# Kernel optimization log

Measured on AMD Instinct MI355X. Metric: run time of the kernel, lower is better.

## Reference

```python
import jax, jax.numpy as jnp
import numpy as np

HEADS = 16

def _rope(x):
    # x: (B, H, T, D); rotate pairs (even, odd) along last dim, positions along axis 2
    B, H, T, D = x.shape
    half = D // 2
    theta = 10000.0 ** (-jnp.arange(half, dtype=x.dtype) / half)          # (half,)
    angles = jnp.arange(T, dtype=x.dtype)[:, None] * theta                # (T, half)
    sin, cos = jnp.sin(angles), jnp.cos(angles)                           # (T, half)
    x1, x2 = x[..., ::2], x[..., 1::2]                                    # (B,H,T,half)
    rot = jnp.stack([x1 * cos - x2 * sin, x1 * sin + x2 * cos], axis=-1)  # (B,H,T,half,2)
    return rot.reshape(B, H, T, D)

def setup_inputs() -> dict:
    key = jax.random.key(0)
    k1, k2, k3 = jax.random.split(key, 3)
    B, T, C = 2, 2048, 1024
    return {
        "x": jax.random.normal(k1, (B, T, C), dtype=jnp.float32),
        "W_qkv": jax.random.normal(k2, (3 * C, C), dtype=jnp.float32) * 0.02,
        "W_out": jax.random.normal(k3, (C, C), dtype=jnp.float32) * 0.02,
        "window": 256,
    }

def reference(x, W_qkv, W_out, window):
    B, T, C = x.shape
    H = HEADS
    D = C // H
    # fused QKV projection (torch Linear: y = x @ W.T)
    qkv = jnp.einsum('btc,fc->btf', x, W_qkv)            # (B,T,3C)
    qkv = qkv.reshape(B, T, H, 3 * D).transpose(0, 2, 1, 3)  # (B,H,T,3D)
    q, k, v = jnp.split(qkv, 3, axis=-1)                 # each (B,H,T,D)
    q, k = _rope(q), _rope(k)
    # causal + local-window boolean mask: allow j in [i-window, i]
    i = jnp.arange(T)[:, None]
    j = jnp.arange(T)[None, :]
    mask = (j <= i) & (j >= i - window)                  # (T,T) bool
    scale = 1.0 / jnp.sqrt(jnp.asarray(D, dtype=x.dtype))
    scores = jnp.einsum('bhqd,bhkd->bhqk', q, k) * scale # (B,H,T,T)
    scores = jnp.where(mask[None, None], scores, -jnp.inf)
    attn = jax.nn.softmax(scores, axis=-1)
    out = jnp.einsum('bhqk,bhkd->bhqd', attn, v)         # (B,H,T,D)
    out = out.transpose(0, 2, 1, 3).reshape(B, T, C)
    return jnp.einsum('btc,oc->bto', out, W_out)
```

## Files before the change

### kernel.cpp

```cpp
#include <hip/hip_runtime.h>

typedef float f32x4 __attribute__((ext_vector_type(4)));
typedef __bf16 bf16x8 __attribute__((ext_vector_type(8)));
typedef unsigned short u16x4 __attribute__((ext_vector_type(4)));

__device__ __forceinline__ unsigned short f2bf(float f) {
  union { float f; unsigned int u; } v; v.f = f;
  unsigned int r = (v.u + 0x7FFFu + ((v.u >> 16) & 1u)) >> 16;
  return (unsigned short)r;
}
__device__ __forceinline__ float bf2f(unsigned short h) {
  union { unsigned int u; float f; } v; v.u = ((unsigned int)h) << 16;
  return v.f;
}
__device__ __forceinline__ void gload_lds16(const void* g, void* l) {
  __builtin_amdgcn_global_load_lds(
      (const __attribute__((address_space(1))) unsigned int*)g,
      (__attribute__((address_space(3))) unsigned int*)l, 16, 0, 0);
}

__global__ __launch_bounds__(256) void f2bf_kernel(const float* __restrict__ in,
                                                   unsigned short* __restrict__ out,
                                                   int n4) {
  int i = blockIdx.x * 256 + threadIdx.x;
  if (i < n4) {
    float4 v = ((const float4*)in)[i];
    u16x4 o;
    o.x = f2bf(v.x); o.y = f2bf(v.y); o.z = f2bf(v.z); o.w = f2bf(v.w);
    ((u16x4*)out)[i] = o;
  }
}

template <bool OUTBF16>
__global__ __launch_bounds__(256) void gemm_bt(const unsigned short* __restrict__ A,
                                               const unsigned short* __restrict__ B,
                                               void* __restrict__ C,
                                               int M, int N, int K) {
  __shared__ unsigned short As[128][32];
  __shared__ unsigned short Bs[128][32];
  const int tid = threadIdx.x;
  const int lane = tid & 63;
  const int w = tid >> 6, wr = w >> 1, wc = w & 1;
  const int bm = blockIdx.y * 128, bn = blockIdx.x * 128;
  const int t4 = tid >> 2, c8 = (tid & 3) * 8;
  const unsigned short* Ab = A + (size_t)(bm + t4) * K + c8;
  const unsigned short* Bb = B + (size_t)(bn + t4) * K + c8;
  const int rq = lane & 15, kg = (lane >> 4) * 8;
  f32x4 acc[4][4] = {};
  for (int kt = 0; kt < K; kt += 32) {
    gload_lds16(Ab + kt,                  &As[t4][c8]);
    gload_lds16(Ab + kt + (size_t)64 * K, &As[t4 + 64][c8]);
    gload_lds16(Bb + kt,                  &Bs[t4][c8]);
    gload_lds16(Bb + kt + (size_t)64 * K, &Bs[t4 + 64][c8]);
    __syncthreads();
    bf16x8 fa[4], fb[4];
#pragma unroll
    for (int m = 0; m < 4; ++m) fa[m] = *(const bf16x8*)&As[wr * 64 + m * 16 + rq][kg];
#pragma unroll
    for (int n = 0; n < 4; ++n) fb[n] = *(const bf16x8*)&Bs[wc * 64 + n * 16 + rq][kg];
#pragma unroll
    for (int m = 0; m < 4; ++m)
#pragma unroll
      for (int n = 0; n < 4; ++n)
        acc[m][n] = __builtin_amdgcn_mfma_f32_16x16x32_bf16(fa[m], fb[n], acc[m][n], 0, 0, 0);
    __syncthreads();
  }
  const int r0 = bm + wr * 64 + (lane >> 4) * 4;
  const int c0 = bn + wc * 64 + rq;
#pragma unroll
  for (int m = 0; m < 4; ++m)
#pragma unroll
    for (int n = 0; n < 4; ++n)
#pragma unroll
      for (int j = 0; j < 4; ++j) {
        int row = r0 + m * 16 + j, col = c0 + n * 16;
        if (OUTBF16)
          ((unsigned short*)C)[(size_t)row * N + col] = f2bf(acc[m][n][j]);
        else
          ((float*)C)[(size_t)row * N + col] = acc[m][n][j];
      }
}

__global__ __launch_bounds__(256) void rope_inplace(unsigned short* __restrict__ qkv) {
  int idx = blockIdx.x * 256 + threadIdx.x;
  int dp = idx & 31;
  int t  = (idx >> 5) & 2047;
  int bh = idx >> 16;
  int b = bh >> 4, h = bh & 15;
  unsigned short* p = qkv + (size_t)(b * 2048 + t) * 3072 + h * 192 + dp * 2;
  float theta = exp2f(-(float)dp * 0.4152410118609203f);
  float ang = (float)t * theta;
  float sn, cs;
  sincosf(ang, &sn, &cs);
  float q1 = bf2f(p[0]), q2 = bf2f(p[1]);
  p[0] = f2bf(q1 * cs - q2 * sn);
  p[1] = f2bf(q1 * sn + q2 * cs);
  float k1 = bf2f(p[64]), k2 = bf2f(p[65]);
  p[64] = f2bf(k1 * cs - k2 * sn);
  p[65] = f2bf(k1 * sn + k2 * cs);
}

#define WMAX 256
__global__ __launch_bounds__(256) void attn_kernel(const unsigned short* __restrict__ qkv,
                                                   unsigned short* __restrict__ attnb,
                                                   const int* __restrict__ winp) {
  __shared__ unsigned short Qs[64][72];
  __shared__ unsigned short KPs[320 * 72];
  __shared__ unsigned short Vt[64][328];
  const int T = 2048;
  const int tid = threadIdx.x;
  const int bid = blockIdx.x;
  const int qt = bid & 31;
  const int bh = bid >> 5;
  const int b = bh >> 4, h = bh & 15;
  const int qbase = qt * 64;
  const int kbase = qbase - WMAX;
  const int win = *winp;
  const unsigned short* base = qkv + (size_t)b * T * 3072 + h * 192;
  const int tr = tid >> 2, tc = (tid & 3) * 16;
  {
    const unsigned short* s = base + (size_t)(qbase + tr) * 3072 + tc;
    *(int4*)&Qs[tr][tc]     = *(const int4*)s;
    *(int4*)&Qs[tr][tc + 8] = *(const int4*)(s + 8);
  }
#pragma unroll
  for (int p5 = 0; p5 < 5; ++p5) {
    int s = p5 * 64 + tr;
    int j = kbase + s;
    int jc = j < 0 ? 0 : j;
    const unsigned short* sk = base + (size_t)jc * 3072 + 64 + tc;
    *(int4*)&KPs[s * 72 + tc]     = *(const int4*)sk;
    *(int4*)&KPs[s * 72 + tc + 8] = *(const int4*)(sk + 8);
    const unsigned short* sv = base + (size_t)jc * 3072 + 128 + tc;
    unsigned short tmp[16];
    *(int4*)&tmp[0] = *(const int4*)sv;
    *(int4*)&tmp[8] = *(const int4*)(sv + 8);
#pragma unroll
    for (int e = 0; e < 16; ++e) Vt[tc + e][s] = tmp[e];
  }
  __syncthreads();
  const int lane = tid & 63, wv = tid >> 6;
  const int rbase = wv * 16;
  const int rq = lane & 15, kg = (lane >> 4) * 8;
  bf16x8 qa[2];
#pragma unroll
  for (int kk = 0; kk < 2; ++kk)
    qa[kk] = *(const bf16x8*)&Qs[rbase + rq][kk * 32 + kg];
  float sc[20][4];
#pragma unroll
  for (int n = 0; n < 20; ++n) {
    f32x4 s = {};
#pragma unroll
    for (int kk = 0; kk < 2; ++kk) {
      bf16x8 kb = *(const bf16x8*)&KPs[(n * 16 + rq) * 72 + kk * 32 + kg];
      s = __builtin_amdgcn_mfma_f32_16x16x32_bf16(qa[kk], kb, s, 0, 0, 0);
    }
#pragma unroll
    for (int r = 0; r < 4; ++r) sc[n][r] = s[r];
  }
  const float scale = 0.125f;
#pragma unroll
  for (int r = 0; r < 4; ++r) {
    const int i = qbase + rbase + (lane >> 4) * 4 + r;
    float mx = -1e30f;
#pragma unroll
    for (int n = 0; n < 20; ++n) {
      int j = kbase + n * 16 + rq;
      bool valid = (j >= 0) && (j <= i) && (i - j <= win);
      float v = valid ? sc[n][r] * scale : -1e30f;
      sc[n][r] = v;
      mx = fmaxf(mx, v);
    }
#pragma unroll
    for (int off = 1; off < 16; off <<= 1) mx = fmaxf(mx, __shfl_xor(mx, off));
    float sum = 0.f;
#pragma unroll
    for (int n = 0; n < 20; ++n) {
      float pv = __expf(sc[n][r] - mx);
      sc[n][r] = pv;
      sum += pv;
    }
#pragma unroll
    for (int off = 1; off < 16; off <<= 1) sum += __shfl_xor(sum, off);
    float inv = 1.0f / sum;
#pragma unroll
    for (int n = 0; n < 20; ++n) sc[n][r] *= inv;
  }
  __syncthreads();
#pragma unroll
  for (int n = 0; n < 20; ++n)
#pragma unroll
    for (int r = 0; r < 4; ++r)
      KPs[(rbase + (lane >> 4) * 4 + r) * 328 + n * 16 + rq] = f2bf(sc[n][r]);
  f32x4 oacc[4] = {};
#pragma unroll
  for (int kk = 0; kk < 10; ++kk) {
    bf16x8 pa = *(const bf16x8*)&KPs[(rbase + rq) * 328 + kk * 32 + kg];
#pragma unroll
    for (int n = 0; n < 4; ++n) {
      bf16x8 vb = *(const bf16x8*)&Vt[n * 16 + rq][kk * 32 + kg];
      oacc[n] = __builtin_amdgcn_mfma_f32_16x16x32_bf16(pa, vb, oacc[n], 0, 0, 0);
    }
  }
#pragma unroll
  for (int n = 0; n < 4; ++n)
#pragma unroll
    for (int j = 0; j < 4; ++j) {
      int r = qbase + rbase + (lane >> 4) * 4 + j;
      int d = n * 16 + rq;
      attnb[(size_t)(b * T + r) * 1024 + h * 64 + d] = f2bf(oacc[n][j]);
    }
}

extern "C" void kernel_launch(void* const* d_in, const int* in_sizes, int n_in,
                              void* d_out, int out_size, void* d_ws, size_t ws_size,
                              hipStream_t stream) {
  const float* x    = (const float*)d_in[0];
  const float* Wqkv = (const float*)d_in[1];
  const float* Wout = (const float*)d_in[2];
  const int*   winp = (const int*)d_in[3];

  const int M = 4096;
  const int C = 1024;
  const int N1 = 3072;
  unsigned short* xb    = (unsigned short*)d_ws;
  unsigned short* wqkvb = xb    + (size_t)M * C;
  unsigned short* woutb = wqkvb + (size_t)N1 * C;
  unsigned short* qkvb  = woutb + (size_t)C * C;
  unsigned short* attnb = qkvb  + (size_t)M * N1;

  f2bf_kernel<<<(M * C / 4 + 255) / 256, 256, 0, stream>>>(x, xb, M * C / 4);
  f2bf_kernel<<<(N1 * C / 4 + 255) / 256, 256, 0, stream>>>(Wqkv, wqkvb, N1 * C / 4);
  f2bf_kernel<<<(C * C / 4 + 255) / 256, 256, 0, stream>>>(Wout, woutb, C * C / 4);

  dim3 g1(N1 / 128, M / 128);
  gemm_bt<true><<<g1, 256, 0, stream>>>(xb, wqkvb, qkvb, M, N1, C);

  rope_inplace<<<(2 * 16 * 2048 * 32) / 256, 256, 0, stream>>>(qkvb);

  attn_kernel<<<2 * 16 * 32, 256, 0, stream>>>(qkvb, attnb, winp);

  dim3 g2(C / 128, M / 128);
  gemm_bt<false><<<g2, 256, 0, stream>>>(attnb, woutb, (float*)d_out, M, C, C);
}
```

Baseline: 196.1 us.

## Fuse RoPE into QKV GEMM epilogue, merge conversions, and pipeline GEMM

The three fp32-to-bf16 conversion launches become one prep kernel, which also fills a cos/sin table for RoPE. The QKV projection moves to a new 128x256-tile GEMM with 512 threads, a three-stage global_load_lds pipeline and XOR-swizzled LDS. RoPE is applied in its epilogue by exchanging lane pairs with shuffles, which removes the separate in-place rope pass over the QKV buffer. It costs more LDS per block, lowers occupancy (launch bounds 512,1) and adds table lookups to the epilogue.

```diff
diff --git a/kernel.cpp b/kernel.cpp
--- a/kernel.cpp
+++ b/kernel.cpp
@@ -19,16 +19,132 @@
       (__attribute__((address_space(3))) unsigned int*)l, 16, 0, 0);
 }
 
-__global__ __launch_bounds__(256) void f2bf_kernel(const float* __restrict__ in,
-                                                   unsigned short* __restrict__ out,
-                                                   int n4) {
-  int i = blockIdx.x * 256 + threadIdx.x;
-  if (i < n4) {
-    float4 v = ((const float4*)in)[i];
+__global__ __launch_bounds__(256) void prep_kernel(
+    const float* __restrict__ x, const float* __restrict__ wqkv,
+    const float* __restrict__ wout, unsigned short* __restrict__ xb,
+    unsigned short* __restrict__ wqkvb, unsigned short* __restrict__ woutb,
+    float2* __restrict__ tab) {
+  const int N1 = 1048576, N2 = 786432, N3 = 262144;
+  int idx = blockIdx.x * 256 + threadIdx.x;
+  if (idx < N1 + N2 + N3) {
+    const float* src; unsigned short* dst; int i = idx;
+    if (i < N1)           { src = x;    dst = xb; }
+    else if (i < N1 + N2) { i -= N1;      src = wqkv; dst = wqkvb; }
+    else                  { i -= N1 + N2; src = wout; dst = woutb; }
+    float4 v = ((const float4*)src)[i];
     u16x4 o;
     o.x = f2bf(v.x); o.y = f2bf(v.y); o.z = f2bf(v.z); o.w = f2bf(v.w);
-    ((u16x4*)out)[i] = o;
-  }
+    ((u16x4*)dst)[i] = o;
+  } else {
+    int i = idx - (N1 + N2 + N3);
+    if (i < 65536) {
+      int t = i >> 5, p = i & 31;
+      float theta = exp2f(-(float)p * 0.4152410118609203f);
+      float sn, cs;
+      sincosf((float)t * theta, &sn, &cs);
+      tab[i] = make_float2(cs, sn);
+    }
+  }
+}
+
+#define G1_SLOT ((128 + 256) * 64)
+
+__global__ __launch_bounds__(512, 1) void gemm1_qkv(
+    const unsigned short* __restrict__ A,
+    const unsigned short* __restrict__ B,
+    unsigned short* __restrict__ Cq,
+    const float2* __restrict__ tab) {
+  __shared__ unsigned short lds[3 * G1_SLOT];
+  const int K = 1024, NJ = 3072, NT = 16;
+  const int tid = threadIdx.x;
+  const int bm = blockIdx.y * 128, bn = blockIdx.x * 256;
+  const int lane = tid & 63, w = tid >> 6, wr = w >> 2, wc = w & 3;
+  const int rq = lane & 15, hi = lane >> 4;
+
+  auto stage = [&](int slot, int kt) {
+    unsigned short* s = lds + slot * G1_SLOT;
+#pragma unroll
+    for (int p = 0; p < 2; ++p) {
+      int ch = tid + p * 512;
+      int row = ch >> 3, blk = (ch & 7) ^ (row & 7);
+      gload_lds16(A + (size_t)(bm + row) * K + kt + blk * 8, s + ch * 8);
+    }
+#pragma unroll
+    for (int p = 0; p < 4; ++p) {
+      int ch = tid + p * 512;
+      int row = ch >> 3, blk = (ch & 7) ^ (row & 7);
+      gload_lds16(B + (size_t)(bn + row) * K + kt + blk * 8,
+                  s + 128 * 64 + ch * 8);
+    }
+  };
+
+  f32x4 acc[4][4] = {};
+  auto compute = [&](int slot) {
+    const unsigned short* sA = lds + slot * G1_SLOT;
+    const unsigned short* sB = sA + 128 * 64;
+#pragma unroll
+    for (int k = 0; k < 2; ++k) {
+      bf16x8 fa[4], fb[4];
+#pragma unroll
+      for (int m = 0; m < 4; ++m) {
+        int r = wr * 64 + m * 16 + rq;
+        int b = (hi + k * 4) ^ (r & 7);
+        fa[m] = *(const bf16x8*)(sA + r * 64 + b * 8);
+      }
+#pragma unroll
+      for (int n = 0; n < 4; ++n) {
+        int r = wc * 64 + n * 16 + rq;
+        int b = (hi + k * 4) ^ (r & 7);
+        fb[n] = *(const bf16x8*)(sB + r * 64 + b * 8);
+      }
+#pragma unroll
+      for (int m = 0; m < 4; ++m)
+#pragma unroll
+        for (int n = 0; n < 4; ++n)
+          acc[m][n] = __builtin_amdgcn_mfma_f32_16x16x32_bf16(fa[m], fb[n], acc[m][n], 0, 0, 0);
+    }
+  };
+
+  stage(0, 0);
+  stage(1, 64);
+  for (int t = 0; t < NT; ++t) {
+    asm volatile("s_waitcnt lgkmcnt(0)" ::: "memory");
+    __builtin_amdgcn_s_barrier();
+    if (t + 2 < NT) stage((t + 2) % 3, (t + 2) * 64);
+    if (t < NT - 2)
+      asm volatile("s_waitcnt vmcnt(12)" ::: "memory");
+    else if (t == NT - 2)
+      asm volatile("s_waitcnt vmcnt(6)" ::: "memory");
+    else
+      asm volatile("s_waitcnt vmcnt(0)" ::: "memory");
+    __builtin_amdgcn_s_barrier();
+    compute(t % 3);
+  }
+
+  const int r0 = bm + wr * 64 + hi * 4;
+  const int c0 = bn + wc * 64 + rq;
+#pragma unroll
+  for (int m = 0; m < 4; ++m)
+#pragma unroll
+    for (int n = 0; n < 4; ++n) {
+      int col = c0 + n * 16;
+      int cw = col % 192;
+      bool dorot = cw < 128;
+      int p = (cw & 63) >> 1;
+#pragma unroll
+      for (int j = 0; j < 4; ++j) {
+        int row = r0 + m * 16 + j;
+        float val = acc[m][n][j];
+        float part = __shfl_xor(val, 1);
+        float outv = val;
+        if (dorot) {
+          float2 cssn = tab[(row & 2047) * 32 + p];
+          outv = (col & 1) ? (part * cssn.y + val * cssn.x)
+                           : (val * cssn.x - part * cssn.y);
+        }
+        Cq[(size_t)row * NJ + col] = f2bf(outv);
+      }
+    }
 }
 
 template <bool OUTBF16>
@@ -81,25 +197,6 @@
       }
 }
 
-__global__ __launch_bounds__(256) void rope_inplace(unsigned short* __restrict__ qkv) {
-  int idx = blockIdx.x * 256 + threadIdx.x;
-  int dp = idx & 31;
-  int t  = (idx >> 5) & 2047;
-  int bh = idx >> 16;
-  int b = bh >> 4, h = bh & 15;
-  unsigned short* p = qkv + (size_t)(b * 2048 + t) * 3072 + h * 192 + dp * 2;
-  float theta = exp2f(-(float)dp * 0.4152410118609203f);
-  float ang = (float)t * theta;
-  float sn, cs;
-  sincosf(ang, &sn, &cs);
-  float q1 = bf2f(p[0]), q2 = bf2f(p[1]);
-  p[0] = f2bf(q1 * cs - q2 * sn);
-  p[1] = f2bf(q1 * sn + q2 * cs);
-  float k1 = bf2f(p[64]), k2 = bf2f(p[65]);
-  p[64] = f2bf(k1 * cs - k2 * sn);
-  p[65] = f2bf(k1 * sn + k2 * cs);
-}
-
 #define WMAX 256
 __global__ __launch_bounds__(256) void attn_kernel(const unsigned short* __restrict__ qkv,
                                                    unsigned short* __restrict__ attnb,
@@ -220,23 +317,19 @@
   const float* Wout = (const float*)d_in[2];
   const int*   winp = (const int*)d_in[3];
 
-  const int M = 4096;
-  const int C = 1024;
-  const int N1 = 3072;
+  const int M = 4096, C = 1024, N1 = 3072;
   unsigned short* xb    = (unsigned short*)d_ws;
   unsigned short* wqkvb = xb    + (size_t)M * C;
   unsigned short* woutb = wqkvb + (size_t)N1 * C;
   unsigned short* qkvb  = woutb + (size_t)C * C;
   unsigned short* attnb = qkvb  + (size_t)M * N1;
-
-  f2bf_kernel<<<(M * C / 4 + 255) / 256, 256, 0, stream>>>(x, xb, M * C / 4);
-  f2bf_kernel<<<(N1 * C / 4 + 255) / 256, 256, 0, stream>>>(Wqkv, wqkvb, N1 * C / 4);
-  f2bf_kernel<<<(C * C / 4 + 255) / 256, 256, 0, stream>>>(Wout, woutb, C * C / 4);
-
-  dim3 g1(N1 / 128, M / 128);
-  gemm_bt<true><<<g1, 256, 0, stream>>>(xb, wqkvb, qkvb, M, N1, C);
-
-  rope_inplace<<<(2 * 16 * 2048 * 32) / 256, 256, 0, stream>>>(qkvb);
+  float2*         tab   = (float2*)(attnb + (size_t)M * C);
+
+  const int PREP = 1048576 + 786432 + 262144 + 65536;
+  prep_kernel<<<(PREP + 255) / 256, 256, 0, stream>>>(x, Wqkv, Wout, xb, wqkvb,
+                                                      woutb, tab);
+
+  gemm1_qkv<<<dim3(12, 32), 512, 0, stream>>>(xb, wqkvb, qkvb, tab);
 
   attn_kernel<<<2 * 16 * 32, 256, 0, stream>>>(qkvb, attnb, winp);
 
```

Result: slower. 214.3 us (+9.3%).
